# Kernel optimization log

Measured on AMD Instinct MI355X. Metric: run time of the kernel, lower is better.

## Reference

```python
import jax, jax.numpy as jnp
import numpy as np

N_NODES = 100000
N_EDGES = 1000000


def gcn_conv(x, W, b, src, dst, n_nodes):
    """PyG GCNConv: add self-loops, symmetric deg^{-1/2} norm, scatter-add."""
    loop = jnp.arange(n_nodes, dtype=src.dtype)
    s = jnp.concatenate([src, loop])
    d = jnp.concatenate([dst, loop])
    deg = jax.ops.segment_sum(jnp.ones_like(d, dtype=x.dtype), d, num_segments=n_nodes)
    dinv = jnp.where(deg > 0, jax.lax.rsqrt(deg), 0.0)
    norm = dinv[s] * dinv[d]  # [E+N]
    h = x @ W                  # transform before propagate (PyG order)
    msg = h[s] * norm[:, None]
    out = jax.ops.segment_sum(msg, d, num_segments=n_nodes)
    return out + b


def setup_inputs() -> dict:
    key = jax.random.key(0)
    ks = jax.random.split(key, 10)
    x = jax.random.normal(ks[0], (N_NODES, 500), dtype=jnp.float32)
    edge_index = jax.random.randint(ks[1], (2, N_EDGES), 0, N_NODES, dtype=jnp.int64 if jax.config.jax_enable_x64 else jnp.int32).astype(jnp.int32)
    W1 = jax.random.normal(ks[2], (500, 256), dtype=jnp.float32) * (1.0 / np.sqrt(500))
    b1 = jax.random.normal(ks[3], (256,), dtype=jnp.float32) * 0.01
    W2 = jax.random.normal(ks[4], (256, 64), dtype=jnp.float32) * (1.0 / np.sqrt(256))
    b2 = jax.random.normal(ks[5], (64,), dtype=jnp.float32) * 0.01
    WB = jax.random.normal(ks[6], (64, 1), dtype=jnp.float32) * (1.0 / 8.0)
    bB = jax.random.normal(ks[7], (1,), dtype=jnp.float32) * 0.01
    WW = jax.random.normal(ks[8], (64, 1), dtype=jnp.float32) * (1.0 / 8.0)
    bW = jax.random.normal(ks[9], (1,), dtype=jnp.float32) * 0.01
    return {"x": x, "edge_index": edge_index, "W1": W1, "b1": b1, "W2": W2,
            "b2": b2, "WB": WB, "bB": bB, "WW": WW, "bW": bW}


def reference(x, edge_index, W1, b1, W2, b2, WB, bB, WW, bW):
    src, dst = edge_index[0], edge_index[1]
    h = gcn_conv(x, W1, b1, src, dst, N_NODES)
    h = jax.nn.relu(h)  # dropout is identity in eval mode
    h = gcn_conv(h, W2, b2, src, dst, N_NODES)
    h = jax.nn.relu(h)
    biases = h @ WB + bB  # [N, 1]
    s2, d2 = src[::2], dst[::2]  # every other edge
    ew = (h[s2] + h[d2]) * 0.5   # [E//2, 64]
    weights = ew @ WW + bW       # [E//2, 1]
    return (weights, biases)
```

## Files before the change

### kernel.cpp

```cpp
#include <hip/hip_runtime.h>
#include <hip/hip_bf16.h>
#include <math.h>

#define NN 100000
#define NE 1000000

typedef __attribute__((ext_vector_type(8))) short bf16x8;
typedef __attribute__((ext_vector_type(4))) float f32x4;

__device__ __forceinline__ unsigned short f2bf(float f) {
    unsigned int u = __builtin_bit_cast(unsigned int, f);
    unsigned int r = (u + 0x7fff + ((u >> 16) & 1)) >> 16;
    return (unsigned short)r;
}
__device__ __forceinline__ float bf2f(unsigned short s) {
    unsigned int u = ((unsigned int)s) << 16;
    return __builtin_bit_cast(float, u);
}


__global__ void count_kernel(const int* __restrict__ dst, int* __restrict__ cnt, int n) {
    int e = blockIdx.x * blockDim.x + threadIdx.x;
    if (e < n) atomicAdd(&cnt[dst[e]], 1);
}

__global__ void dinv_kernel(const int* __restrict__ cnt, float* __restrict__ dinv, int n) {
    int v = blockIdx.x * blockDim.x + threadIdx.x;
    if (v < n) dinv[v] = 1.0f / sqrtf((float)cnt[v] + 1.0f);
}

__global__ void scan1_kernel(const int* __restrict__ cnt, int* __restrict__ tmp,
                             int* __restrict__ bsum, int n) {
    __shared__ int sh[1024];
    int t = threadIdx.x;
    int i = blockIdx.x * 1024 + t;
    int v = (i < n) ? cnt[i] : 0;
    sh[t] = v;
    __syncthreads();
    for (int off = 1; off < 1024; off <<= 1) {
        int a = (t >= off) ? sh[t - off] : 0;
        __syncthreads();
        sh[t] += a;
        __syncthreads();
    }
    if (i < n) tmp[i] = sh[t];
    if (t == 1023) bsum[blockIdx.x] = sh[t];
}

__global__ void scan2_kernel(int* __restrict__ bsum, int nb) {
    __shared__ int sh[128];
    int t = threadIdx.x;
    int v = (t < nb) ? bsum[t] : 0;
    sh[t] = v;
    __syncthreads();
    for (int off = 1; off < 128; off <<= 1) {
        int a = (t >= off) ? sh[t - off] : 0;
        __syncthreads();
        sh[t] += a;
        __syncthreads();
    }
    if (t < nb) bsum[t] = sh[t] - v;
}

__global__ void scan3_kernel(const int* __restrict__ tmp, const int* __restrict__ cnt,
                             const int* __restrict__ bsum, int* __restrict__ rp, int n) {
    int i = blockIdx.x * 1024 + threadIdx.x;
    if (i < n) {
        int base = bsum[blockIdx.x];
        rp[i] = base + tmp[i] - cnt[i];
        if (i == n - 1) rp[n] = base + tmp[i];
    }
}

__global__ void fill_kernel(const int* __restrict__ src, const int* __restrict__ dst,
                            const int* __restrict__ rp, int* __restrict__ fill,
                            int* __restrict__ csrc, int n) {
    int e = blockIdx.x * blockDim.x + threadIdx.x;
    if (e < n) {
        int d = dst[e];
        int pos = rp[d] + atomicAdd(&fill[d], 1);
        csrc[pos] = src[e];
    }
}

__global__ void convW1t_kernel(const float* __restrict__ W1, unsigned short* __restrict__ W1t) {
    int i = blockIdx.x * blockDim.x + threadIdx.x;
    if (i < 256 * 512) {
        int n = i >> 9, k = i & 511;
        W1t[i] = (k < 500) ? f2bf(W1[(size_t)k * 256 + n]) : (unsigned short)0;
    }
}

__global__ void convW2t_kernel(const float* __restrict__ W2, unsigned short* __restrict__ W2t) {
    int i = blockIdx.x * blockDim.x + threadIdx.x;
    if (i < 64 * 256) {
        int n = i >> 8, k = i & 255;
        W2t[i] = f2bf(W2[(size_t)k * 64 + n]);
    }
}

#define G1_BM 128
#define G1_BN 256
#define G1_BK 64

__launch_bounds__(512)
__global__ void gemm1_mfma(const float* __restrict__ A,
                           const unsigned short* __restrict__ Bt,
                           unsigned short* __restrict__ C,
                           int M) {
    __shared__ char lds[(G1_BM + G1_BN) * G1_BK * 2];
    char* As = lds;
    char* Bs = lds + G1_BM * G1_BK * 2;
    const int t = threadIdx.x;
    const int l = t & 63;
    const int w = t >> 6;
    const int wr = w >> 2;
    const int wc = w & 3;
    const int bm = blockIdx.x * G1_BM;

    f32x4 acc[4][4] = {};

    for (int k0 = 0; k0 < 512; k0 += G1_BK) {
#pragma unroll
        for (int j = 0; j < 2; j++) {
            int c = j * 512 + t;
            int row = c >> 3, slot = c & 7;
            int R = bm + row;
            int kbase = k0 + slot * 8;
            float f[8];
            if (R < M && kbase + 8 <= 500) {
                float4 u0 = *(const float4*)(A + (size_t)R * 500 + kbase);
                float4 u1 = *(const float4*)(A + (size_t)R * 500 + kbase + 4);
                f[0] = u0.x; f[1] = u0.y; f[2] = u0.z; f[3] = u0.w;
                f[4] = u1.x; f[5] = u1.y; f[6] = u1.z; f[7] = u1.w;
            } else {
#pragma unroll
                for (int i = 0; i < 8; i++) {
                    int k = kbase + i;
                    f[i] = (R < M && k < 500) ? A[(size_t)R * 500 + k] : 0.f;
                }
            }
            union { uint4 u; unsigned short s[8]; } pk;
#pragma unroll
            for (int i = 0; i < 8; i++) pk.s[i] = f2bf(f[i]);
            *(uint4*)(As + row * 128 + ((slot ^ (row & 7)) * 16)) = pk.u;
        }
#pragma unroll
        for (int j = 0; j < 4; j++) {
            int c = j * 512 + t;
            int col = c >> 3, slot = c & 7;
            uint4 v = *(const uint4*)(Bt + (size_t)col * 512 + k0 + slot * 8);
            *(uint4*)(Bs + col * 128 + ((slot ^ (col & 7)) * 16)) = v;
        }
        __syncthreads();
#pragma unroll
        for (int kk = 0; kk < 2; kk++) {
            bf16x8 af[4], bg[4];
#pragma unroll
            for (int m = 0; m < 4; m++) {
                int row = wr * 64 + m * 16 + (l & 15);
                int slot = kk * 4 + (l >> 4);
                af[m] = *(const bf16x8*)(As + row * 128 + ((slot ^ (row & 7)) * 16));
            }
#pragma unroll
            for (int n = 0; n < 4; n++) {
                int col = wc * 64 + n * 16 + (l & 15);
                int slot = kk * 4 + (l >> 4);
                bg[n] = *(const bf16x8*)(Bs + col * 128 + ((slot ^ (col & 7)) * 16));
            }
#pragma unroll
            for (int m = 0; m < 4; m++)
#pragma unroll
                for (int n = 0; n < 4; n++)
                    acc[m][n] = __builtin_amdgcn_mfma_f32_16x16x32_bf16(af[m], bg[n], acc[m][n], 0, 0, 0);
        }
        __syncthreads();
    }
#pragma unroll
    for (int m = 0; m < 4; m++) {
#pragma unroll
        for (int j = 0; j < 4; j++) {
            int row = bm + wr * 64 + m * 16 + (l >> 4) * 4 + j;
            if (row < M) {
#pragma unroll
                for (int n = 0; n < 4; n++) {
                    int col = wc * 64 + n * 16 + (l & 15);
                    C[(size_t)row * 256 + col] = f2bf(acc[m][n][j]);
                }
            }
        }
    }
}

__global__ void agg1_kernel(const unsigned short* __restrict__ h, const float* __restrict__ dinv,
                            const int* __restrict__ rp, const int* __restrict__ csrc,
                            const float* __restrict__ bias, unsigned short* __restrict__ out, int n) {
    int wave = (blockIdx.x * blockDim.x + threadIdx.x) >> 6;
    int lane = threadIdx.x & 63;
    if (wave >= n) return;
    int v = wave;
    float dv = dinv[v];
    ushort4 sv = ((const ushort4*)(h + (size_t)v * 256))[lane];
    float a0 = bf2f(sv.x) * dv, a1 = bf2f(sv.y) * dv, a2 = bf2f(sv.z) * dv, a3 = bf2f(sv.w) * dv;
    int b0 = rp[v], b1e = rp[v + 1];
    for (int i = b0; i < b1e; i++) {
        int s = csrc[i];
        float ds = dinv[s];
        ushort4 hs = ((const ushort4*)(h + (size_t)s * 256))[lane];
        a0 += bf2f(hs.x) * ds; a1 += bf2f(hs.y) * ds;
        a2 += bf2f(hs.z) * ds; a3 += bf2f(hs.w) * ds;
    }
    float4 bb = ((const float4*)bias)[lane];
    ushort4 ov;
    ov.x = f2bf(fmaxf(a0 * dv + bb.x, 0.f));
    ov.y = f2bf(fmaxf(a1 * dv + bb.y, 0.f));
    ov.z = f2bf(fmaxf(a2 * dv + bb.z, 0.f));
    ov.w = f2bf(fmaxf(a3 * dv + bb.w, 0.f));
    ((ushort4*)(out + (size_t)v * 256))[lane] = ov;
}

#define G2_BM 256
#define G2_BN 64
#define G2_BK 64

__launch_bounds__(512)
__global__ void gemm2_mfma(const unsigned short* __restrict__ A,
                           const unsigned short* __restrict__ Bt,
                           float* __restrict__ C,
                           int M) {
    __shared__ char lds[(G2_BM + G2_BN) * G2_BK * 2];
    char* As = lds;
    char* Bs = lds + G2_BM * G2_BK * 2;
    const int t = threadIdx.x;
    const int l = t & 63;
    const int w = t >> 6;
    const int bm = blockIdx.x * G2_BM;

    f32x4 acc[2][4] = {};

    for (int k0 = 0; k0 < 256; k0 += G2_BK) {
#pragma unroll
        for (int j = 0; j < 4; j++) {
            int c = j * 512 + t;
            int row = c >> 3, slot = c & 7;
            int R = bm + row;
            uint4 v = {0, 0, 0, 0};
            if (R < M) v = *(const uint4*)(A + (size_t)R * 256 + k0 + slot * 8);
            *(uint4*)(As + row * 128 + ((slot ^ (row & 7)) * 16)) = v;
        }
        {
            int col = t >> 3, slot = t & 7;
            uint4 v = *(const uint4*)(Bt + (size_t)col * 256 + k0 + slot * 8);
            *(uint4*)(Bs + col * 128 + ((slot ^ (col & 7)) * 16)) = v;
        }
        __syncthreads();
#pragma unroll
        for (int kk = 0; kk < 2; kk++) {
            bf16x8 af[2], bg[4];
#pragma unroll
            for (int m = 0; m < 2; m++) {
                int row = w * 32 + m * 16 + (l & 15);
                int slot = kk * 4 + (l >> 4);
                af[m] = *(const bf16x8*)(As + row * 128 + ((slot ^ (row & 7)) * 16));
            }
#pragma unroll
            for (int n = 0; n < 4; n++) {
                int col = n * 16 + (l & 15);
                int slot = kk * 4 + (l >> 4);
                bg[n] = *(const bf16x8*)(Bs + col * 128 + ((slot ^ (col & 7)) * 16));
            }
#pragma unroll
            for (int m = 0; m < 2; m++)
#pragma unroll
                for (int n = 0; n < 4; n++)
                    acc[m][n] = __builtin_amdgcn_mfma_f32_16x16x32_bf16(af[m], bg[n], acc[m][n], 0, 0, 0);
        }
        __syncthreads();
    }
#pragma unroll
    for (int m = 0; m < 2; m++) {
#pragma unroll
        for (int j = 0; j < 4; j++) {
            int row = bm + w * 32 + m * 16 + (l >> 4) * 4 + j;
            if (row < M) {
#pragma unroll
                for (int n = 0; n < 4; n++) {
                    int col = n * 16 + (l & 15);
                    C[(size_t)row * 64 + col] = acc[m][n][j];
                }
            }
        }
    }
}

__global__ void agg2_kernel(const float* __restrict__ h, const float* __restrict__ dinv,
                            const int* __restrict__ rp, const int* __restrict__ csrc,
                            const float* __restrict__ bias, float* __restrict__ out, int n) {
    int wave = (blockIdx.x * blockDim.x + threadIdx.x) >> 6;
    int lane = threadIdx.x & 63;
    if (wave >= n) return;
    int v = wave;
    float dv = dinv[v];
    float acc = h[(size_t)v * 64 + lane] * dv;
    int b0 = rp[v], b1e = rp[v + 1];
    for (int i = b0; i < b1e; i++) {
        int s = csrc[i];
        acc += h[(size_t)s * 64 + lane] * dinv[s];
    }
    out[(size_t)v * 64 + lane] = fmaxf(acc * dv + bias[lane], 0.f);
}

__global__ void heads_kernel(const float* __restrict__ h, const float* __restrict__ WW,
                             const float* __restrict__ WB, const float* __restrict__ bB,
                             float* __restrict__ p, float* __restrict__ outB, int n) {
    int wave = (blockIdx.x * blockDim.x + threadIdx.x) >> 6;
    int lane = threadIdx.x & 63;
    if (wave >= n) return;
    int v = wave;
    float hv = h[(size_t)v * 64 + lane];
    float pw = hv * WW[lane];
    float pb = hv * WB[lane];
#pragma unroll
    for (int off = 32; off >= 1; off >>= 1) {
        pw += __shfl_xor(pw, off);
        pb += __shfl_xor(pb, off);
    }
    if (lane == 0) {
        p[v] = pw;
        outB[v] = pb + bB[0];
    }
}

__global__ void weights_kernel(const int* __restrict__ src, const int* __restrict__ dst,
                               const float* __restrict__ p, const float* __restrict__ bW,
                               float* __restrict__ outW, int n) {
    int i = blockIdx.x * blockDim.x + threadIdx.x;
    if (i < n) {
        int e = 2 * i;
        outW[i] = 0.5f * (p[src[e]] + p[dst[e]]) + bW[0];
    }
}


extern "C" void kernel_launch(void* const* d_in, const int* in_sizes, int n_in,
                              void* d_out, int out_size, void* d_ws, size_t ws_size,
                              hipStream_t stream) {
    const float* x  = (const float*)d_in[0];
    const int*   ei = (const int*)d_in[1];
    const int*   src = ei;
    const int*   dst = ei + NE;
    const float* W1 = (const float*)d_in[2];
    const float* b1 = (const float*)d_in[3];
    const float* W2 = (const float*)d_in[4];
    const float* b2 = (const float*)d_in[5];
    const float* WB = (const float*)d_in[6];
    const float* bB = (const float*)d_in[7];
    const float* WW = (const float*)d_in[8];
    const float* bW = (const float*)d_in[9];
    float* outW = (float*)d_out;
    float* outB = (float*)d_out + 500000;

    char* ws = (char*)d_ws;
    unsigned short* h1b = (unsigned short*)(ws);
    unsigned short* h1a = (unsigned short*)(ws + 51200000);
    float* h2  = (float*)(ws);
    float* h2a = (float*)(ws + 25600000);
    float* p   = (float*)(ws + 153600000);
    char* tail = ws + 155000000;
    float* dinv = (float*)(tail);
    int*   rp   = (int*)(tail + 400000);
    int*   cnt  = (int*)(tail + 800064);
    int*   fill = (int*)(tail + 1200064);
    int*   csrc = (int*)(tail + 1600064);
    int*   tmp  = (int*)(tail + 5600064);
    int*   bsum = (int*)(tail + 6000064);
    unsigned short* W1t = (unsigned short*)(tail + 6000576);
    unsigned short* W2t = (unsigned short*)(tail + 6524864);

    hipMemsetAsync(cnt, 0, 800000, stream);

    count_kernel<<<(NE + 255) / 256, 256, 0, stream>>>(dst, cnt, NE);
    dinv_kernel<<<(NN + 255) / 256, 256, 0, stream>>>(cnt, dinv, NN);
    int nblk = (NN + 1023) / 1024;
    scan1_kernel<<<nblk, 1024, 0, stream>>>(cnt, tmp, bsum, NN);
    scan2_kernel<<<1, 128, 0, stream>>>(bsum, nblk);
    scan3_kernel<<<nblk, 1024, 0, stream>>>(tmp, cnt, bsum, rp, NN);
    fill_kernel<<<(NE + 255) / 256, 256, 0, stream>>>(src, dst, rp, fill, csrc, NE);

    convW1t_kernel<<<(256 * 512 + 255) / 256, 256, 0, stream>>>(W1, W1t);
    convW2t_kernel<<<(64 * 256 + 255) / 256, 256, 0, stream>>>(W2, W2t);
    gemm1_mfma<<<(NN + G1_BM - 1) / G1_BM, 512, 0, stream>>>(x, W1t, h1b, NN);
    agg1_kernel<<<(NN + 3) / 4, 256, 0, stream>>>(h1b, dinv, rp, csrc, b1, h1a, NN);

    gemm2_mfma<<<(NN + G2_BM - 1) / G2_BM, 512, 0, stream>>>(h1a, W2t, h2, NN);
    agg2_kernel<<<(NN + 3) / 4, 256, 0, stream>>>(h2, dinv, rp, csrc, b2, h2a, NN);

    heads_kernel<<<(NN + 3) / 4, 256, 0, stream>>>(h2a, WW, WB, bB, p, outB, NN);
    weights_kernel<<<(500000 + 255) / 256, 256, 0, stream>>>(src, dst, p, bW, outW, 500000);
}
```

Measured before the change: 699.0 us.

## Prefetch GEMM tiles into registers, unroll gathers, fuse agg2 with heads

Both MFMA GEMMs now load the next K-tile from global memory into registers while MFMAs run on the current LDS tile, then write it to LDS after a barrier. The aggregation loops are unrolled by four so several neighbour-row gathers are in flight at once. The second aggregation is fused with the heads kernel, which removes the h2a intermediate write and re-read plus one launch. The cost is higher register pressure and an extra barrier per K iteration in the GEMMs.

```diff
diff --git a/kernel.cpp b/kernel.cpp
--- a/kernel.cpp
+++ b/kernel.cpp
@@ -102,6 +102,58 @@
 #define G1_BM 128
 #define G1_BN 256
 #define G1_BK 64
+
+__device__ __forceinline__ void g1_loadA(const float* __restrict__ A, int bm, int M, int t,
+                                         int k0, float (&fr)[2][8]) {
+#pragma unroll
+    for (int j = 0; j < 2; j++) {
+        int c = j * 512 + t;
+        int row = c >> 3, slot = c & 7;
+        int R = bm + row;
+        int kbase = k0 + slot * 8;
+        if (R < M && kbase + 8 <= 500) {
+            float4 u0 = *(const float4*)(A + (size_t)R * 500 + kbase);
+            float4 u1 = *(const float4*)(A + (size_t)R * 500 + kbase + 4);
+            fr[j][0] = u0.x; fr[j][1] = u0.y; fr[j][2] = u0.z; fr[j][3] = u0.w;
+            fr[j][4] = u1.x; fr[j][5] = u1.y; fr[j][6] = u1.z; fr[j][7] = u1.w;
+        } else {
+#pragma unroll
+            for (int i = 0; i < 8; i++) {
+                int k = kbase + i;
+                fr[j][i] = (R < M && k < 500) ? A[(size_t)R * 500 + k] : 0.f;
+            }
+        }
+    }
+}
+
+__device__ __forceinline__ void g1_loadB(const unsigned short* __restrict__ Bt, int t,
+                                         int k0, uint4 (&vb)[4]) {
+#pragma unroll
+    for (int j = 0; j < 4; j++) {
+        int c = j * 512 + t;
+        int col = c >> 3, slot = c & 7;
+        vb[j] = *(const uint4*)(Bt + (size_t)col * 512 + k0 + slot * 8);
+    }
+}
+
+__device__ __forceinline__ void g1_write(char* As, char* Bs, int t,
+                                         const float (&fr)[2][8], const uint4 (&vb)[4]) {
+#pragma unroll
+    for (int j = 0; j < 2; j++) {
+        int c = j * 512 + t;
+        int row = c >> 3, slot = c & 7;
+        union { uint4 u; unsigned short s[8]; } pk;
+#pragma unroll
+        for (int i = 0; i < 8; i++) pk.s[i] = f2bf(fr[j][i]);
+        *(uint4*)(As + row * 128 + ((slot ^ (row & 7)) * 16)) = pk.u;
+    }
+#pragma unroll
+    for (int j = 0; j < 4; j++) {
+        int c = j * 512 + t;
+        int col = c >> 3, slot = c & 7;
+        *(uint4*)(Bs + col * 128 + ((slot ^ (col & 7)) * 16)) = vb[j];
+    }
+}
 
 __launch_bounds__(512)
 __global__ void gemm1_mfma(const float* __restrict__ A,
@@ -119,40 +171,20 @@
     const int bm = blockIdx.x * G1_BM;
 
     f32x4 acc[4][4] = {};
+    float fr[2][8];
+    uint4 vb[4];
+
+    g1_loadA(A, bm, M, t, 0, fr);
+    g1_loadB(Bt, t, 0, vb);
+    g1_write(As, Bs, t, fr, vb);
+    __syncthreads();
 
     for (int k0 = 0; k0 < 512; k0 += G1_BK) {
-#pragma unroll
-        for (int j = 0; j < 2; j++) {
-            int c = j * 512 + t;
-            int row = c >> 3, slot = c & 7;
-            int R = bm + row;
-            int kbase = k0 + slot * 8;
-            float f[8];
-            if (R < M && kbase + 8 <= 500) {
-                float4 u0 = *(const float4*)(A + (size_t)R * 500 + kbase);
-                float4 u1 = *(const float4*)(A + (size_t)R * 500 + kbase + 4);
-                f[0] = u0.x; f[1] = u0.y; f[2] = u0.z; f[3] = u0.w;
-                f[4] = u1.x; f[5] = u1.y; f[6] = u1.z; f[7] = u1.w;
-            } else {
-#pragma unroll
-                for (int i = 0; i < 8; i++) {
-                    int k = kbase + i;
-                    f[i] = (R < M && k < 500) ? A[(size_t)R * 500 + k] : 0.f;
-                }
-            }
-            union { uint4 u; unsigned short s[8]; } pk;
-#pragma unroll
-            for (int i = 0; i < 8; i++) pk.s[i] = f2bf(f[i]);
-            *(uint4*)(As + row * 128 + ((slot ^ (row & 7)) * 16)) = pk.u;
-        }
-#pragma unroll
-        for (int j = 0; j < 4; j++) {
-            int c = j * 512 + t;
-            int col = c >> 3, slot = c & 7;
-            uint4 v = *(const uint4*)(Bt + (size_t)col * 512 + k0 + slot * 8);
-            *(uint4*)(Bs + col * 128 + ((slot ^ (col & 7)) * 16)) = v;
-        }
-        __syncthreads();
+        int kn = k0 + G1_BK;
+        if (kn < 512) {
+            g1_loadA(A, bm, M, t, kn, fr);
+            g1_loadB(Bt, t, kn, vb);
+        }
 #pragma unroll
         for (int kk = 0; kk < 2; kk++) {
             bf16x8 af[4], bg[4];
@@ -173,6 +205,10 @@
 #pragma unroll
                 for (int n = 0; n < 4; n++)
                     acc[m][n] = __builtin_amdgcn_mfma_f32_16x16x32_bf16(af[m], bg[n], acc[m][n], 0, 0, 0);
+        }
+        __syncthreads();
+        if (kn < 512) {
+            g1_write(As, Bs, t, fr, vb);
         }
         __syncthreads();
     }
@@ -203,7 +239,20 @@
     ushort4 sv = ((const ushort4*)(h + (size_t)v * 256))[lane];
     float a0 = bf2f(sv.x) * dv, a1 = bf2f(sv.y) * dv, a2 = bf2f(sv.z) * dv, a3 = bf2f(sv.w) * dv;
     int b0 = rp[v], b1e = rp[v + 1];
-    for (int i = b0; i < b1e; i++) {
+    int i = b0;
+    for (; i + 4 <= b1e; i += 4) {
+        int s0 = csrc[i], s1 = csrc[i + 1], s2 = csrc[i + 2], s3 = csrc[i + 3];
+        float d0 = dinv[s0], d1 = dinv[s1], d2 = dinv[s2], d3 = dinv[s3];
+        ushort4 r0 = ((const ushort4*)(h + (size_t)s0 * 256))[lane];
+        ushort4 r1 = ((const ushort4*)(h + (size_t)s1 * 256))[lane];
+        ushort4 r2 = ((const ushort4*)(h + (size_t)s2 * 256))[lane];
+        ushort4 r3 = ((const ushort4*)(h + (size_t)s3 * 256))[lane];
+        a0 += bf2f(r0.x) * d0 + bf2f(r1.x) * d1 + bf2f(r2.x) * d2 + bf2f(r3.x) * d3;
+        a1 += bf2f(r0.y) * d0 + bf2f(r1.y) * d1 + bf2f(r2.y) * d2 + bf2f(r3.y) * d3;
+        a2 += bf2f(r0.z) * d0 + bf2f(r1.z) * d1 + bf2f(r2.z) * d2 + bf2f(r3.z) * d3;
+        a3 += bf2f(r0.w) * d0 + bf2f(r1.w) * d1 + bf2f(r2.w) * d2 + bf2f(r3.w) * d3;
+    }
+    for (; i < b1e; i++) {
         int s = csrc[i];
         float ds = dinv[s];
         ushort4 hs = ((const ushort4*)(h + (size_t)s * 256))[lane];
@@ -222,6 +271,32 @@
 #define G2_BM 256
 #define G2_BN 64
 #define G2_BK 64
+
+__device__ __forceinline__ void g2_loadA(const unsigned short* __restrict__ A, int bm, int M,
+                                         int t, int k0, uint4 (&va)[4]) {
+#pragma unroll
+    for (int j = 0; j < 4; j++) {
+        int c = j * 512 + t;
+        int row = c >> 3, slot = c & 7;
+        int R = bm + row;
+        uint4 z = {0, 0, 0, 0};
+        va[j] = (R < M) ? *(const uint4*)(A + (size_t)R * 256 + k0 + slot * 8) : z;
+    }
+}
+
+__device__ __forceinline__ void g2_write(char* As, char* Bs, int t,
+                                         const uint4 (&va)[4], const uint4& vbv) {
+#pragma unroll
+    for (int j = 0; j < 4; j++) {
+        int c = j * 512 + t;
+        int row = c >> 3, slot = c & 7;
+        *(uint4*)(As + row * 128 + ((slot ^ (row & 7)) * 16)) = va[j];
+    }
+    {
+        int col = t >> 3, slot = t & 7;
+        *(uint4*)(Bs + col * 128 + ((slot ^ (col & 7)) * 16)) = vbv;
+    }
+}
 
 __launch_bounds__(512)
 __global__ void gemm2_mfma(const unsigned short* __restrict__ A,
@@ -237,23 +312,19 @@
     const int bm = blockIdx.x * G2_BM;
 
     f32x4 acc[2][4] = {};
+    uint4 va[4], vbv;
+
+    g2_loadA(A, bm, M, t, 0, va);
+    vbv = *(const uint4*)(Bt + (size_t)(t >> 3) * 256 + (t & 7) * 8);
+    g2_write(As, Bs, t, va, vbv);
+    __syncthreads();
 
     for (int k0 = 0; k0 < 256; k0 += G2_BK) {
-#pragma unroll
-        for (int j = 0; j < 4; j++) {
-            int c = j * 512 + t;
-            int row = c >> 3, slot = c & 7;
-            int R = bm + row;
-            uint4 v = {0, 0, 0, 0};
-            if (R < M) v = *(const uint4*)(A + (size_t)R * 256 + k0 + slot * 8);
-            *(uint4*)(As + row * 128 + ((slot ^ (row & 7)) * 16)) = v;
-        }
-        {
-            int col = t >> 3, slot = t & 7;
-            uint4 v = *(const uint4*)(Bt + (size_t)col * 256 + k0 + slot * 8);
-            *(uint4*)(Bs + col * 128 + ((slot ^ (col & 7)) * 16)) = v;
-        }
-        __syncthreads();
+        int kn = k0 + G2_BK;
+        if (kn < 256) {
+            g2_loadA(A, bm, M, t, kn, va);
+            vbv = *(const uint4*)(Bt + (size_t)(t >> 3) * 256 + kn + (t & 7) * 8);
+        }
 #pragma unroll
         for (int kk = 0; kk < 2; kk++) {
             bf16x8 af[2], bg[4];
@@ -276,6 +347,10 @@
                     acc[m][n] = __builtin_amdgcn_mfma_f32_16x16x32_bf16(af[m], bg[n], acc[m][n], 0, 0, 0);
         }
         __syncthreads();
+        if (kn < 256) {
+            g2_write(As, Bs, t, va, vbv);
+        }
+        __syncthreads();
     }
 #pragma unroll
     for (int m = 0; m < 2; m++) {
@@ -293,9 +368,12 @@
     }
 }
 
-__global__ void agg2_kernel(const float* __restrict__ h, const float* __restrict__ dinv,
-                            const int* __restrict__ rp, const int* __restrict__ csrc,
-                            const float* __restrict__ bias, float* __restrict__ out, int n) {
+__global__ void agg2heads_kernel(const float* __restrict__ h, const float* __restrict__ dinv,
+                                 const int* __restrict__ rp, const int* __restrict__ csrc,
+                                 const float* __restrict__ bias,
+                                 const float* __restrict__ WW, const float* __restrict__ WB,
+                                 const float* __restrict__ bB,
+                                 float* __restrict__ p, float* __restrict__ outB, int n) {
     int wave = (blockIdx.x * blockDim.x + threadIdx.x) >> 6;
     int lane = threadIdx.x & 63;
     if (wave >= n) return;
@@ -303,21 +381,21 @@
     float dv = dinv[v];
     float acc = h[(size_t)v * 64 + lane] * dv;
     int b0 = rp[v], b1e = rp[v + 1];
-    for (int i = b0; i < b1e; i++) {
+    int i = b0;
+    for (; i + 4 <= b1e; i += 4) {
+        int s0 = csrc[i], s1 = csrc[i + 1], s2 = csrc[i + 2], s3 = csrc[i + 3];
+        float d0 = dinv[s0], d1 = dinv[s1], d2 = dinv[s2], d3 = dinv[s3];
+        float r0 = h[(size_t)s0 * 64 + lane];
+        float r1 = h[(size_t)s1 * 64 + lane];
+        float r2 = h[(size_t)s2 * 64 + lane];
+        float r3 = h[(size_t)s3 * 64 + lane];
+        acc += r0 * d0 + r1 * d1 + r2 * d2 + r3 * d3;
+    }
+    for (; i < b1e; i++) {
         int s = csrc[i];
         acc += h[(size_t)s * 64 + lane] * dinv[s];
     }
-    out[(size_t)v * 64 + lane] = fmaxf(acc * dv + bias[lane], 0.f);
-}
-
-__global__ void heads_kernel(const float* __restrict__ h, const float* __restrict__ WW,
-                             const float* __restrict__ WB, const float* __restrict__ bB,
-                             float* __restrict__ p, float* __restrict__ outB, int n) {
-    int wave = (blockIdx.x * blockDim.x + threadIdx.x) >> 6;
-    int lane = threadIdx.x & 63;
-    if (wave >= n) return;
-    int v = wave;
-    float hv = h[(size_t)v * 64 + lane];
+    float hv = fmaxf(acc * dv + bias[lane], 0.f);
     float pw = hv * WW[lane];
     float pb = hv * WB[lane];
 #pragma unroll
@@ -364,7 +442,6 @@
     unsigned short* h1b = (unsigned short*)(ws);
     unsigned short* h1a = (unsigned short*)(ws + 51200000);
     float* h2  = (float*)(ws);
-    float* h2a = (float*)(ws + 25600000);
     float* p   = (float*)(ws + 153600000);
     char* tail = ws + 155000000;
     float* dinv = (float*)(tail);
@@ -393,8 +470,7 @@
     agg1_kernel<<<(NN + 3) / 4, 256, 0, stream>>>(h1b, dinv, rp, csrc, b1, h1a, NN);
 
     gemm2_mfma<<<(NN + G2_BM - 1) / G2_BM, 512, 0, stream>>>(h1a, W2t, h2, NN);
-    agg2_kernel<<<(NN + 3) / 4, 256, 0, stream>>>(h2, dinv, rp, csrc, b2, h2a, NN);
-
-    heads_kernel<<<(NN + 3) / 4, 256, 0, stream>>>(h2a, WW, WB, bB, p, outB, NN);
+    agg2heads_kernel<<<(NN + 3) / 4, 256, 0, stream>>>(h2, dinv, rp, csrc, b2, WW, WB, bB, p, outB, NN);
+
     weights_kernel<<<(500000 + 255) / 256, 256, 0, stream>>>(src, dst, p, bW, outW, 500000);
 }
```

After: 661.8 us. 5.3% less time.
